# Performance work log

Hardware: AMD Instinct MI355X
Metric: run time of the kernel (lower is better)

The kernel has to match this reference:

```python
import jax, jax.numpy as jnp
import numpy as np
from jax import lax

NUM_EXPERTS = 64
HIDDEN = 1024
INTERMEDIATE = 768
TOTAL_TOKENS = 8192


def setup_inputs() -> dict:
    key = jax.random.key(0)
    k1, k2, k3, k4 = jax.random.split(key, 4)
    x = jax.random.normal(k1, (TOTAL_TOKENS, HIDDEN), dtype=jnp.float32)
    scale = 0.02
    w1 = jax.random.normal(k2, (NUM_EXPERTS, HIDDEN, INTERMEDIATE), dtype=jnp.float32) * scale
    w2 = jax.random.normal(k3, (NUM_EXPERTS, INTERMEDIATE, HIDDEN), dtype=jnp.float32) * scale
    w3 = jax.random.normal(k4, (NUM_EXPERTS, HIDDEN, INTERMEDIATE), dtype=jnp.float32) * scale
    # Variable tokens per expert, summing exactly to TOTAL_TOKENS (tokens are pre-sorted by expert).
    counts = np.random.default_rng(0).multinomial(TOTAL_TOKENS, [1.0 / NUM_EXPERTS] * NUM_EXPERTS)
    num_tokens_per_expert = jnp.asarray(counts, dtype=jnp.int32)
    return {"x": x, "w1": w1, "w2": w2, "w3": w3,
            "num_tokens_per_expert": num_tokens_per_expert}


def reference(x, w1, w2, w3, num_tokens_per_expert):
    """SwiGLU grouped-expert FFN: down(silu(gate(x)) * up(x)), grouped by expert.

    x: (T, H) tokens sorted by expert; num_tokens_per_expert: (E,) int32.
    Matches torch._grouped_mm semantics: compute in bfloat16, cast back to x.dtype.
    """
    gs = num_tokens_per_expert.astype(jnp.int32)
    xb = x.astype(jnp.bfloat16)
    w1b = w1.astype(jnp.bfloat16)
    w2b = w2.astype(jnp.bfloat16)
    w3b = w3.astype(jnp.bfloat16)
    gate = lax.ragged_dot(xb, w1b, gs)          # (T, I) grouped GEMM
    up = lax.ragged_dot(xb, w3b, gs)            # (T, I)
    h = jax.nn.silu(gate) * up                  # fused SwiGLU activation
    out = lax.ragged_dot(h, w2b, gs)            # (T, H)
    return out.astype(x.dtype)
```

## Files before the change

kernel.cpp:

```cpp
#include <hip/hip_runtime.h>
#include <stdint.h>

#define E_ 64
#define H_ 1024
#define I_ 768
#define T_ 8192

typedef __attribute__((ext_vector_type(4))) float floatx4;
typedef __attribute__((ext_vector_type(8))) short bf16x8;

__device__ inline unsigned short f2bf(float f) {
  union { float f; uint32_t u; } v; v.f = f;
  return (unsigned short)((v.u + 0x7FFFu + ((v.u >> 16) & 1u)) >> 16);
}
__device__ inline float bf2f(unsigned short s) {
  union { uint32_t u; float f; } v; v.u = ((uint32_t)s) << 16;
  return v.f;
}

__device__ inline void gload16(const void* g, void* l) {
  __builtin_amdgcn_global_load_lds(
      (const __attribute__((address_space(1))) void*)g,
      (__attribute__((address_space(3))) void*)l, 16, 0, 0);
}

__global__ void k_prep(const float* __restrict__ x, unsigned short* __restrict__ xb,
                       const int* __restrict__ cnts, int* __restrict__ offs) {
  int i = blockIdx.x * 256 + threadIdx.x;
  float4 v = ((const float4*)x)[i];
  ushort4 o;
  o.x = f2bf(v.x); o.y = f2bf(v.y); o.z = f2bf(v.z); o.w = f2bf(v.w);
  ((ushort4*)xb)[i] = o;
  if (i == 0) {
    int s = 0; offs[0] = 0;
    for (int e = 0; e < E_; ++e) { s += cnts[e]; offs[e + 1] = s; }
  }
}

__global__ __launch_bounds__(256, 2) void k_gemm1(
    const unsigned short* __restrict__ xb, const float* __restrict__ w1,
    const float* __restrict__ w3, unsigned short* __restrict__ h,
    const int* __restrict__ offs) {
  __shared__ unsigned short As[256 * 32];
  __shared__ float Bs1[32 * 64];
  __shared__ float Bs3[32 * 64];

  const int tid = threadIdx.x;
  const int wv = tid >> 6;
  const int l = tid & 63;
  const int lq = l >> 4;
  const int ln = l & 15;
  const int e = blockIdx.x / (I_ / 64);
  const int n0 = (blockIdx.x % (I_ / 64)) * 64;
  const int off = offs[e];
  const int cnt = offs[e + 1] - off;

  const float* b1p = w1 + (size_t)e * (H_ * I_) + (size_t)(tid >> 4) * I_ + n0 + (tid & 15) * 4;
  const float* b3p = w3 + (size_t)e * (H_ * I_) + (size_t)(tid >> 4) * I_ + n0 + (tid & 15) * 4;
  unsigned short* aDst = &As[tid * 8];
  float* b1Dst = &Bs1[tid * 4];
  float* b3Dst = &Bs3[tid * 4];

  for (int mb = 0; mb < cnt; mb += 256) {
    const int m_here = (cnt - mb) < 256 ? (cnt - mb) : 256;
    const bool active = (wv * 64) < m_here;

    const unsigned short* aptr[4];
#pragma unroll
    for (int r = 0; r < 4; ++r) {
      int row = off + mb + r * 64 + (tid >> 2);
      row = row < (T_ - 1) ? row : (T_ - 1);
      aptr[r] = xb + (size_t)row * H_ + (tid & 3) * 8;
    }

    floatx4 accG[4][4], accU[4][4];
#pragma unroll
    for (int i2 = 0; i2 < 4; ++i2)
#pragma unroll
      for (int j2 = 0; j2 < 4; ++j2) {
        accG[i2][j2] = (floatx4){0.f, 0.f, 0.f, 0.f};
        accU[i2][j2] = (floatx4){0.f, 0.f, 0.f, 0.f};
      }

    for (int kt = 0; kt < H_ / 32; ++kt) {
      __syncthreads();
#pragma unroll
      for (int r = 0; r < 4; ++r)
        gload16(aptr[r] + kt * 32, aDst + r * 2048);
#pragma unroll
      for (int r = 0; r < 2; ++r) {
        gload16(b1p + (size_t)(kt * 32 + r * 16) * I_, b1Dst + r * 1024);
        gload16(b3p + (size_t)(kt * 32 + r * 16) * I_, b3Dst + r * 1024);
      }
      __syncthreads();

      if (active) {
        bf16x8 bG[4], bU[4];
#pragma unroll
        for (int nf = 0; nf < 4; ++nf) {
          const float* p1 = &Bs1[(lq * 8) * 64 + nf * 16 + ln];
          const float* p3 = &Bs3[(lq * 8) * 64 + nf * 16 + ln];
          bf16x8 t1, t3;
#pragma unroll
          for (int j = 0; j < 8; ++j) {
            t1[j] = (short)f2bf(p1[j * 64]);
            t3[j] = (short)f2bf(p3[j * 64]);
          }
          bG[nf] = t1; bU[nf] = t3;
        }
#pragma unroll
        for (int mf = 0; mf < 4; ++mf) {
          const bf16x8 af = *(const bf16x8*)&As[(size_t)(wv * 64 + mf * 16 + ln) * 32 + lq * 8];
#pragma unroll
          for (int nf = 0; nf < 4; ++nf) {
            accG[mf][nf] = __builtin_amdgcn_mfma_f32_16x16x32_bf16(af, bG[nf], accG[mf][nf], 0, 0, 0);
            accU[mf][nf] = __builtin_amdgcn_mfma_f32_16x16x32_bf16(af, bU[nf], accU[mf][nf], 0, 0, 0);
          }
        }
      }
    }

    if (active) {
#pragma unroll
      for (int mf = 0; mf < 4; ++mf)
#pragma unroll
        for (int nf = 0; nf < 4; ++nf)
#pragma unroll
          for (int r = 0; r < 4; ++r) {
            int row_l = wv * 64 + mf * 16 + lq * 4 + r;
            if (row_l < m_here) {
              float g = bf2f(f2bf(accG[mf][nf][r]));
              float u = bf2f(f2bf(accU[mf][nf][r]));
              float hv = (g / (1.0f + __expf(-g))) * u;
              h[(size_t)(off + mb + row_l) * I_ + n0 + nf * 16 + ln] = f2bf(hv);
            }
          }
    }
  }
}

__global__ __launch_bounds__(256, 2) void k_gemm2(
    const unsigned short* __restrict__ h, const float* __restrict__ w2,
    float* __restrict__ out, const int* __restrict__ offs) {
  __shared__ unsigned short As[256 * 32];
  __shared__ float Bs[32 * 64];

  const int tid = threadIdx.x;
  const int wv = tid >> 6;
  const int l = tid & 63;
  const int lq = l >> 4;
  const int ln = l & 15;
  const int e = blockIdx.x / (H_ / 64);
  const int n0 = (blockIdx.x % (H_ / 64)) * 64;
  const int off = offs[e];
  const int cnt = offs[e + 1] - off;

  const float* b2p = w2 + (size_t)e * (I_ * H_) + (size_t)(tid >> 4) * H_ + n0 + (tid & 15) * 4;
  unsigned short* aDst = &As[tid * 8];
  float* bDst = &Bs[tid * 4];

  for (int mb = 0; mb < cnt; mb += 256) {
    const int m_here = (cnt - mb) < 256 ? (cnt - mb) : 256;
    const bool active = (wv * 64) < m_here;

    const unsigned short* aptr[4];
#pragma unroll
    for (int r = 0; r < 4; ++r) {
      int row = off + mb + r * 64 + (tid >> 2);
      row = row < (T_ - 1) ? row : (T_ - 1);
      aptr[r] = h + (size_t)row * I_ + (tid & 3) * 8;
    }

    floatx4 acc[4][4];
#pragma unroll
    for (int i2 = 0; i2 < 4; ++i2)
#pragma unroll
      for (int j2 = 0; j2 < 4; ++j2) acc[i2][j2] = (floatx4){0.f, 0.f, 0.f, 0.f};

    for (int kt = 0; kt < I_ / 32; ++kt) {
      __syncthreads();
#pragma unroll
      for (int r = 0; r < 4; ++r)
        gload16(aptr[r] + kt * 32, aDst + r * 2048);
#pragma unroll
      for (int r = 0; r < 2; ++r)
        gload16(b2p + (size_t)(kt * 32 + r * 16) * H_, bDst + r * 1024);
      __syncthreads();

      if (active) {
        bf16x8 bF[4];
#pragma unroll
        for (int nf = 0; nf < 4; ++nf) {
          const float* p = &Bs[(lq * 8) * 64 + nf * 16 + ln];
          bf16x8 t;
#pragma unroll
          for (int j = 0; j < 8; ++j) t[j] = (short)f2bf(p[j * 64]);
          bF[nf] = t;
        }
#pragma unroll
        for (int mf = 0; mf < 4; ++mf) {
          const bf16x8 af = *(const bf16x8*)&As[(size_t)(wv * 64 + mf * 16 + ln) * 32 + lq * 8];
#pragma unroll
          for (int nf = 0; nf < 4; ++nf)
            acc[mf][nf] = __builtin_amdgcn_mfma_f32_16x16x32_bf16(af, bF[nf], acc[mf][nf], 0, 0, 0);
        }
      }
    }

    if (active) {
#pragma unroll
      for (int mf = 0; mf < 4; ++mf)
#pragma unroll
        for (int nf = 0; nf < 4; ++nf)
#pragma unroll
          for (int r = 0; r < 4; ++r) {
            int row_l = wv * 64 + mf * 16 + lq * 4 + r;
            if (row_l < m_here)
              out[(size_t)(off + mb + row_l) * H_ + n0 + nf * 16 + ln] = acc[mf][nf][r];
          }
    }
  }
}

extern "C" void kernel_launch(void* const* d_in, const int* in_sizes, int n_in,
                              void* d_out, int out_size, void* d_ws, size_t ws_size,
                              hipStream_t stream) {
  const float* x  = (const float*)d_in[0];
  const float* w1 = (const float*)d_in[1];
  const float* w2 = (const float*)d_in[2];
  const float* w3 = (const float*)d_in[3];
  const int* cnts = (const int*)d_in[4];
  float* out = (float*)d_out;

  char* ws = (char*)d_ws;
  int* offs = (int*)ws;
  unsigned short* xb = (unsigned short*)(ws + 1024);
  unsigned short* h  = (unsigned short*)(ws + 1024 + (size_t)T_ * H_ * 2);

  k_prep<<<(T_ * H_) / (256 * 4), 256, 0, stream>>>(x, xb, cnts, offs);
  k_gemm1<<<E_ * (I_ / 64), 256, 0, stream>>>(xb, w1, w3, h, offs);
  k_gemm2<<<E_ * (H_ / 64), 256, 0, stream>>>(h, w2, out, offs);
}
```

Baseline: 645.1 us.

## Double-buffer LDS tiles in both grouped GEMMs to overlap loads with MFMA

```diff
diff --git a/kernel.cpp b/kernel.cpp
--- a/kernel.cpp
+++ b/kernel.cpp
@@ -41,9 +41,9 @@
     const unsigned short* __restrict__ xb, const float* __restrict__ w1,
     const float* __restrict__ w3, unsigned short* __restrict__ h,
     const int* __restrict__ offs) {
-  __shared__ unsigned short As[256 * 32];
-  __shared__ float Bs1[32 * 64];
-  __shared__ float Bs3[32 * 64];
+  __shared__ unsigned short As[2][256 * 32];
+  __shared__ float Bs1[2][32 * 64];
+  __shared__ float Bs3[2][32 * 64];
 
   const int tid = threadIdx.x;
   const int wv = tid >> 6;
@@ -57,9 +57,6 @@
 
   const float* b1p = w1 + (size_t)e * (H_ * I_) + (size_t)(tid >> 4) * I_ + n0 + (tid & 15) * 4;
   const float* b3p = w3 + (size_t)e * (H_ * I_) + (size_t)(tid >> 4) * I_ + n0 + (tid & 15) * 4;
-  unsigned short* aDst = &As[tid * 8];
-  float* b1Dst = &Bs1[tid * 4];
-  float* b3Dst = &Bs3[tid * 4];
 
   for (int mb = 0; mb < cnt; mb += 256) {
     const int m_here = (cnt - mb) < 256 ? (cnt - mb) : 256;
@@ -73,6 +70,17 @@
       aptr[r] = xb + (size_t)row * H_ + (tid & 3) * 8;
     }
 
+    auto STG = [&](int kt, int buf) {
+#pragma unroll
+      for (int r = 0; r < 4; ++r)
+        gload16(aptr[r] + kt * 32, &As[buf][tid * 8 + r * 2048]);
+#pragma unroll
+      for (int r = 0; r < 2; ++r) {
+        gload16(b1p + (size_t)(kt * 32 + r * 16) * I_, &Bs1[buf][tid * 4 + r * 1024]);
+        gload16(b3p + (size_t)(kt * 32 + r * 16) * I_, &Bs3[buf][tid * 4 + r * 1024]);
+      }
+    };
+
     floatx4 accG[4][4], accU[4][4];
 #pragma unroll
     for (int i2 = 0; i2 < 4; ++i2)
@@ -82,24 +90,28 @@
         accU[i2][j2] = (floatx4){0.f, 0.f, 0.f, 0.f};
       }
 
-    for (int kt = 0; kt < H_ / 32; ++kt) {
-      __syncthreads();
-#pragma unroll
-      for (int r = 0; r < 4; ++r)
-        gload16(aptr[r] + kt * 32, aDst + r * 2048);
-#pragma unroll
-      for (int r = 0; r < 2; ++r) {
-        gload16(b1p + (size_t)(kt * 32 + r * 16) * I_, b1Dst + r * 1024);
-        gload16(b3p + (size_t)(kt * 32 + r * 16) * I_, b3Dst + r * 1024);
-      }
-      __syncthreads();
+    const int NK = H_ / 32;
+    STG(0, 0);
+    for (int kt = 0; kt < NK; ++kt) {
+      const int cur = kt & 1;
+      if (kt + 1 < NK) {
+        STG(kt + 1, cur ^ 1);
+        asm volatile("s_waitcnt vmcnt(8)" ::: "memory");
+      } else {
+        asm volatile("s_waitcnt vmcnt(0)" ::: "memory");
+      }
+      __builtin_amdgcn_s_barrier();
+      asm volatile("" ::: "memory");
 
       if (active) {
+        const unsigned short* Asc = As[cur];
+        const float* B1c = Bs1[cur];
+        const float* B3c = Bs3[cur];
         bf16x8 bG[4], bU[4];
 #pragma unroll
         for (int nf = 0; nf < 4; ++nf) {
-          const float* p1 = &Bs1[(lq * 8) * 64 + nf * 16 + ln];
-          const float* p3 = &Bs3[(lq * 8) * 64 + nf * 16 + ln];
+          const float* p1 = &B1c[(lq * 8) * 64 + nf * 16 + ln];
+          const float* p3 = &B3c[(lq * 8) * 64 + nf * 16 + ln];
           bf16x8 t1, t3;
 #pragma unroll
           for (int j = 0; j < 8; ++j) {
@@ -110,7 +122,7 @@
         }
 #pragma unroll
         for (int mf = 0; mf < 4; ++mf) {
-          const bf16x8 af = *(const bf16x8*)&As[(size_t)(wv * 64 + mf * 16 + ln) * 32 + lq * 8];
+          const bf16x8 af = *(const bf16x8*)&Asc[(size_t)(wv * 64 + mf * 16 + ln) * 32 + lq * 8];
 #pragma unroll
           for (int nf = 0; nf < 4; ++nf) {
             accG[mf][nf] = __builtin_amdgcn_mfma_f32_16x16x32_bf16(af, bG[nf], accG[mf][nf], 0, 0, 0);
@@ -118,6 +130,8 @@
           }
         }
       }
+      asm volatile("" ::: "memory");
+      __builtin_amdgcn_s_barrier();
     }
 
     if (active) {
@@ -136,14 +150,15 @@
             }
           }
     }
+    asm volatile("s_waitcnt vmcnt(0)" ::: "memory");
   }
 }
 
-__global__ __launch_bounds__(256, 2) void k_gemm2(
+__global__ __launch_bounds__(256, 3) void k_gemm2(
     const unsigned short* __restrict__ h, const float* __restrict__ w2,
     float* __restrict__ out, const int* __restrict__ offs) {
-  __shared__ unsigned short As[256 * 32];
-  __shared__ float Bs[32 * 64];
+  __shared__ unsigned short As[2][256 * 32];
+  __shared__ float Bs[2][32 * 64];
 
   const int tid = threadIdx.x;
   const int wv = tid >> 6;
@@ -156,8 +171,6 @@
   const int cnt = offs[e + 1] - off;
 
   const float* b2p = w2 + (size_t)e * (I_ * H_) + (size_t)(tid >> 4) * H_ + n0 + (tid & 15) * 4;
-  unsigned short* aDst = &As[tid * 8];
-  float* bDst = &Bs[tid * 4];
 
   for (int mb = 0; mb < cnt; mb += 256) {
     const int m_here = (cnt - mb) < 256 ? (cnt - mb) : 256;
@@ -171,27 +184,41 @@
       aptr[r] = h + (size_t)row * I_ + (tid & 3) * 8;
     }
 
+    auto STG = [&](int kt, int buf) {
+#pragma unroll
+      for (int r = 0; r < 4; ++r)
+        gload16(aptr[r] + kt * 32, &As[buf][tid * 8 + r * 2048]);
+#pragma unroll
+      for (int r = 0; r < 2; ++r)
+        gload16(b2p + (size_t)(kt * 32 + r * 16) * H_, &Bs[buf][tid * 4 + r * 1024]);
+    };
+
     floatx4 acc[4][4];
 #pragma unroll
     for (int i2 = 0; i2 < 4; ++i2)
 #pragma unroll
       for (int j2 = 0; j2 < 4; ++j2) acc[i2][j2] = (floatx4){0.f, 0.f, 0.f, 0.f};
 
-    for (int kt = 0; kt < I_ / 32; ++kt) {
-      __syncthreads();
-#pragma unroll
-      for (int r = 0; r < 4; ++r)
-        gload16(aptr[r] + kt * 32, aDst + r * 2048);
-#pragma unroll
-      for (int r = 0; r < 2; ++r)
-        gload16(b2p + (size_t)(kt * 32 + r * 16) * H_, bDst + r * 1024);
-      __syncthreads();
+    const int NK = I_ / 32;
+    STG(0, 0);
+    for (int kt = 0; kt < NK; ++kt) {
+      const int cur = kt & 1;
+      if (kt + 1 < NK) {
+        STG(kt + 1, cur ^ 1);
+        asm volatile("s_waitcnt vmcnt(6)" ::: "memory");
+      } else {
+        asm volatile("s_waitcnt vmcnt(0)" ::: "memory");
+      }
+      __builtin_amdgcn_s_barrier();
+      asm volatile("" ::: "memory");
 
       if (active) {
+        const unsigned short* Asc = As[cur];
+        const float* Bc = Bs[cur];
         bf16x8 bF[4];
 #pragma unroll
         for (int nf = 0; nf < 4; ++nf) {
-          const float* p = &Bs[(lq * 8) * 64 + nf * 16 + ln];
+          const float* p = &Bc[(lq * 8) * 64 + nf * 16 + ln];
           bf16x8 t;
 #pragma unroll
           for (int j = 0; j < 8; ++j) t[j] = (short)f2bf(p[j * 64]);
@@ -199,12 +226,14 @@
         }
 #pragma unroll
         for (int mf = 0; mf < 4; ++mf) {
-          const bf16x8 af = *(const bf16x8*)&As[(size_t)(wv * 64 + mf * 16 + ln) * 32 + lq * 8];
+          const bf16x8 af = *(const bf16x8*)&Asc[(size_t)(wv * 64 + mf * 16 + ln) * 32 + lq * 8];
 #pragma unroll
           for (int nf = 0; nf < 4; ++nf)
             acc[mf][nf] = __builtin_amdgcn_mfma_f32_16x16x32_bf16(af, bF[nf], acc[mf][nf], 0, 0, 0);
         }
       }
+      asm volatile("" ::: "memory");
+      __builtin_amdgcn_s_barrier();
     }
 
     if (active) {
@@ -219,6 +248,7 @@
               out[(size_t)(off + mb + row_l) * H_ + n0 + nf * 16 + ln] = acc[mf][nf][r];
           }
     }
+    asm volatile("s_waitcnt vmcnt(0)" ::: "memory");
   }
 }
 
```

Result: faster. 628.7 us (-2.5%).
